# Performance work log

Hardware: AMD Instinct MI355X
Metric: run time of the kernel (lower is better)

The kernel has to match this reference:

```python
import jax, jax.numpy as jnp
import numpy as np

N_NODE = 100000
HIDDEN = 128
BATCH = 4096
SESS_LEN = 50


def setup_inputs() -> dict:
    key = jax.random.key(0)
    k1, k2, k3, k4, k5 = jax.random.split(key, 5)
    return {
        "item_embedding": jax.random.normal(k1, (N_NODE, HIDDEN), dtype=jnp.float32),
        "items": jax.random.randint(k2, (BATCH, SESS_LEN), 0, N_NODE, dtype=jnp.int64),
        "A": jax.random.uniform(k3, (BATCH, BATCH), dtype=jnp.float32),
        "D": jax.random.uniform(k4, (BATCH, BATCH), dtype=jnp.float32),
        "target_embedding": jax.random.normal(k5, (BATCH, 1, 2 * HIDDEN), dtype=jnp.float32),
    }


def reference(item_embedding, items, A, D, target_embedding):
    # Gather per-session item embeddings: (batch, sess_len, hidden)
    seq_h = item_embedding[items]
    # Sum over session positions -> (batch, hidden)
    relation_emb = jnp.sum(seq_h, axis=1)
    # DA = D @ A, then propagate: (batch, batch) @ (batch, hidden)
    DA = jnp.matmul(D, A)
    relation_emb = jnp.matmul(DA, relation_emb)
    # Row-wise L2 normalization (torch.norm(dim=-1))
    norm = jnp.linalg.norm(relation_emb, axis=-1, keepdims=True)
    return relation_emb / norm
```

## Files before the change

### kernel.cpp

```cpp
#include <hip/hip_runtime.h>
#include <hip/hip_bf16.h>

#define BATCH   4096
#define HIDDEN  128
#define SESS    50
#define KTOT    4096
#define NB      ((size_t)BATCH * HIDDEN)

#define MROWS   128
#define KSP     8
#define KQL     512
#define BK      32
#define NTL     (KQL / BK)
#define ABY     16384
#define BBY     8192
#define BUF     (ABY + BBY)
#define NBUF    5

typedef __bf16 bf16x8 __attribute__((ext_vector_type(8)));
typedef float  f32x4  __attribute__((ext_vector_type(4)));
typedef float  f32x2  __attribute__((ext_vector_type(2)));

__device__ __forceinline__ f32x4 mfma_bf16(bf16x8 a, bf16x8 b, f32x4 c) {
    return __builtin_amdgcn_mfma_f32_16x16x32_bf16(a, b, c, 0, 0, 0);
}

__device__ __forceinline__ void gload16(const void* g, void* l) {
    __builtin_amdgcn_global_load_lds(
        (const __attribute__((address_space(1))) void*)g,
        (__attribute__((address_space(3))) void*)l, 16, 0, 0);
}


__global__ __launch_bounds__(256)
void gather_sum_kernel(const float* __restrict__ emb,
                       const int* __restrict__ items32,
                       __bf16* __restrict__ ETp) {
    __shared__ int sidx[4][SESS];
    const int t  = threadIdx.x;
    const int b0 = blockIdx.x * 4;
    const bool is64 = (items32[1] | items32[3] | items32[5] | items32[7] |
                       items32[9] | items32[11] | items32[13] | items32[15]) == 0;
    if (t < 4 * SESS) {
        const int w_ = t / SESS, s_ = t % SESS;
        sidx[w_][s_] = is64
            ? (int)((const long long*)items32)[(long)(b0 + w_) * SESS + s_]
            : items32[(b0 + w_) * SESS + s_];
    }
    __syncthreads();
    const int w    = t >> 6;
    const int lane = t & 63;
    const int c    = lane & 31;
    const int h    = lane >> 5;
    f32x4 acc = {0.f, 0.f, 0.f, 0.f};
#pragma unroll
    for (int i = 0; i < 25; ++i) {
        acc += *(const f32x4*)(emb + (long)sidx[w][h + 2 * i] * HIDDEN + c * 4);
    }
#pragma unroll
    for (int j = 0; j < 4; ++j) acc[j] += __shfl_xor(acc[j], 32, 64);
    if (h == 0) {
        const int  b     = b0 + w;
        const long chunk = b >> 3;
        const int  swz   = (int)((chunk & 3) << 4);
        char* basep = (char*)ETp + chunk * 2048 + (b & 7) * 2;
        const int hi4 = (c >> 2) * 256;
#pragma unroll
        for (int j = 0; j < 4; ++j) {
            const int hl = 4 * (c & 3) + j;
            *(__bf16*)(basep + ((hi4 + hl * 16) ^ swz)) = (__bf16)acc[j];
        }
    }
}

__global__ __launch_bounds__(256, 1)
void gemm_mfma_kernel(const float* __restrict__ X,
                      const char* __restrict__ Bpk,
                      float* __restrict__ Tp) {
    __shared__ __align__(16) char lds[NBUF * BUF];
    const int tid  = threadIdx.x;
    const int w    = tid >> 6;
    const int lane = tid & 63;
    const int lo   = lane & 15;
    const int quad = lane >> 4;
    const int rowBase = blockIdx.x * MROWS;
    const int kq      = blockIdx.y;

    const int mh = w & 1;
    const int nh = w >> 1;
    const int akey = (lo & 7) << 4;
    const int bkey = quad << 4;

#define STG(t_, dst_) do {                                                   \
    _Pragma("unroll")                                                        \
    for (int ai_ = 0; ai_ < 4; ++ai_) {                                      \
        const int i_  = 4 * w + ai_;                                         \
        const int rl_ = 8 * i_ + (lane >> 3);          \
        gload16((const char*)X +                                             \
                    ((size_t)(rowBase + rl_) * KTOT + kq * KQL +             \
                     (size_t)(t_) * BK) * 4 +                                \
                    ((((lane & 7) * 16)) ^ ((rl_ & 7) << 4)),                \
                (dst_) + i_ * 1024);                                         \
    }                                                                        \
    _Pragma("unroll")                                                        \
    for (int bi_ = 0; bi_ < 2; ++bi_) {                                      \
        const int j_ = 2 * w + bi_;                                          \
        gload16(Bpk + ((size_t)(kq * 64 + (t_) * 4 + (j_ >> 1))) * 2048 +    \
                    (j_ & 1) * 1024 + lane * 16,                             \
                (dst_) + ABY + j_ * 1024);                                   \
    }                                                                        \
} while (0)

    f32x4 acc[4][4];
#pragma unroll
    for (int i = 0; i < 4; ++i)
#pragma unroll
        for (int j = 0; j < 4; ++j) acc[i][j] = (f32x4){0.f, 0.f, 0.f, 0.f};

#define KTL(cb_) do {                                                        \
    const char* Ab_ = (cb_);                                                 \
    const char* Bb_ = (cb_) + ABY + quad * 2048;                             \
    bf16x8 af_[4];                                                           \
    _Pragma("unroll")                                                        \
    for (int fm_ = 0; fm_ < 4; ++fm_) {                                      \
        const int rr_ = (mh * 64 + fm_ * 16 + lo) * 128;                     \
        const f32x4 a0_ = *(const f32x4*)(Ab_ + rr_ + ((quad * 32) ^ akey)); \
        const f32x4 a1_ =                                                    \
            *(const f32x4*)(Ab_ + rr_ + ((quad * 32 + 16) ^ akey));          \
        af_[fm_][0] = (__bf16)a0_[0]; af_[fm_][1] = (__bf16)a0_[1];          \
        af_[fm_][2] = (__bf16)a0_[2]; af_[fm_][3] = (__bf16)a0_[3];          \
        af_[fm_][4] = (__bf16)a1_[0]; af_[fm_][5] = (__bf16)a1_[1];          \
        af_[fm_][6] = (__bf16)a1_[2]; af_[fm_][7] = (__bf16)a1_[3];          \
    }                                                                        \
    bf16x8 bf_[4];                                                           \
    _Pragma("unroll")                                                        \
    for (int fn_ = 0; fn_ < 4; ++fn_)                                        \
        bf_[fn_] = *(const bf16x8*)(Bb_ +                                    \
            ((((nh * 4 + fn_) * 256) + lo * 16) ^ bkey));                    \
    _Pragma("unroll")                                                        \
    for (int fm_ = 0; fm_ < 4; ++fm_)                                        \
        _Pragma("unroll")                                                    \
        for (int fn_ = 0; fn_ < 4; ++fn_)                                    \
            acc[fm_][fn_] = mfma_bf16(af_[fm_], bf_[fn_], acc[fm_][fn_]);    \
} while (0)

    STG(0, lds + 0 * BUF);
    STG(1, lds + 1 * BUF);
    STG(2, lds + 2 * BUF);
    STG(3, lds + 3 * BUF);

#pragma unroll
    for (int t = 0; t < NTL; ++t) {
        if (t <= NTL - 4)
            asm volatile("s_waitcnt vmcnt(18)" ::: "memory");
        else if (t == NTL - 3)
            asm volatile("s_waitcnt vmcnt(12)" ::: "memory");
        else if (t == NTL - 2)
            asm volatile("s_waitcnt vmcnt(6)" ::: "memory");
        else
            asm volatile("s_waitcnt vmcnt(0)" ::: "memory");
        __builtin_amdgcn_s_barrier();
        __builtin_amdgcn_sched_barrier(0);
        if (t + 4 < NTL) STG(t + 4, lds + ((t + 4) % NBUF) * BUF);
        KTL(lds + (t % NBUF) * BUF);
        __builtin_amdgcn_sched_barrier(0);
    }
#undef STG
#undef KTL

    float* op = Tp + (size_t)kq * NB +
                (size_t)(rowBase + mh * 64) * HIDDEN + nh * 64;
#pragma unroll
    for (int fm = 0; fm < 4; ++fm)
#pragma unroll
        for (int r = 0; r < 4; ++r) {
            const int ro = (fm * 16 + quad * 4 + r) * HIDDEN;
#pragma unroll
            for (int fn = 0; fn < 4; ++fn)
                op[ro + fn * 16 + lo] = acc[fm][fn][r];
        }
}

__global__ __launch_bounds__(256)
void reduce8_kernel(const float* __restrict__ Tp, __bf16* __restrict__ TTp) {
    const size_t i = ((size_t)blockIdx.x * 256 + threadIdx.x) * 4;
    f32x4 a = *(const f32x4*)(Tp + i);
#pragma unroll
    for (int p = 1; p < KSP; ++p) a += *(const f32x4*)(Tp + p * NB + i);
    const int  b     = (int)(i >> 7);
    const int  h0    = (int)(i & 127);
    const long chunk = b >> 3;
    const int  swz   = (int)((chunk & 3) << 4);
    char* basep = (char*)TTp + chunk * 2048 + (b & 7) * 2;
#pragma unroll
    for (int j = 0; j < 4; ++j) {
        const int h = h0 + j;
        *(__bf16*)(basep + (((h >> 4) * 256 + (h & 15) * 16) ^ swz)) =
            (__bf16)a[j];
    }
}

__global__ __launch_bounds__(256)
void rednorm8_kernel(const float* __restrict__ Tp, float* __restrict__ out) {
    const int t    = threadIdx.x;
    const int w    = t >> 6;
    const int lane = t & 63;
    const int row  = blockIdx.x * 4 + w;
    const size_t base = (size_t)row * HIDDEN + lane * 2;
    f32x2 v = *(const f32x2*)(Tp + base);
#pragma unroll
    for (int p = 1; p < KSP; ++p) v += *(const f32x2*)(Tp + p * NB + base);
    float sq = v[0] * v[0] + v[1] * v[1];
#pragma unroll
    for (int m = 1; m < 64; m <<= 1) sq += __shfl_xor(sq, m, 64);
    const float s = rsqrtf(sq);
    f32x2 o = {v[0] * s, v[1] * s};
    *(f32x2*)(out + base) = o;
}

extern "C" void kernel_launch(void* const* d_in, const int* in_sizes, int n_in,
                              void* d_out, int out_size, void* d_ws, size_t ws_size,
                              hipStream_t stream) {
    const float* emb   = (const float*)d_in[0];
    const int*   items = (const int*)d_in[1];
    const float* A     = (const float*)d_in[2];
    const float* D     = (const float*)d_in[3];
    float* out = (float*)d_out;

    __bf16* ETp = (__bf16*)d_ws;
    __bf16* TTp = ETp + NB;
    float*  Tp  = (float*)(TTp + NB);

    gather_sum_kernel<<<BATCH / 4, 256, 0, stream>>>(emb, items, ETp);
    gemm_mfma_kernel<<<dim3(BATCH / MROWS, KSP), 256, 0, stream>>>(
        A, (const char*)ETp, Tp);
    reduce8_kernel<<<512, 256, 0, stream>>>(Tp, TTp);
    gemm_mfma_kernel<<<dim3(BATCH / MROWS, KSP), 256, 0, stream>>>(
        D, (const char*)TTp, Tp);
    rednorm8_kernel<<<BATCH / 4, 256, 0, stream>>>(Tp, out);
}
```

Baseline: 215.0 us.

## Fuse split-K reductions into GEMM kernels via per-row-block atomic counters

```diff
diff --git a/kernel.cpp b/kernel.cpp
--- a/kernel.cpp
+++ b/kernel.cpp
@@ -19,7 +19,6 @@
 
 typedef __bf16 bf16x8 __attribute__((ext_vector_type(8)));
 typedef float  f32x4  __attribute__((ext_vector_type(4)));
-typedef float  f32x2  __attribute__((ext_vector_type(2)));
 
 __device__ __forceinline__ f32x4 mfma_bf16(bf16x8 a, bf16x8 b, f32x4 c) {
     return __builtin_amdgcn_mfma_f32_16x16x32_bf16(a, b, c, 0, 0, 0);
@@ -35,10 +34,12 @@
 __global__ __launch_bounds__(256)
 void gather_sum_kernel(const float* __restrict__ emb,
                        const int* __restrict__ items32,
-                       __bf16* __restrict__ ETp) {
+                       __bf16* __restrict__ ETp,
+                       int* __restrict__ cnt) {
     __shared__ int sidx[4][SESS];
     const int t  = threadIdx.x;
     const int b0 = blockIdx.x * 4;
+    if (blockIdx.x == 0 && t < 64) cnt[t] = 0;
     const bool is64 = (items32[1] | items32[3] | items32[5] | items32[7] |
                        items32[9] | items32[11] | items32[13] | items32[15]) == 0;
     if (t < 4 * SESS) {
@@ -73,18 +74,23 @@
     }
 }
 
+template <int PHASE>
 __global__ __launch_bounds__(256, 1)
 void gemm_mfma_kernel(const float* __restrict__ X,
                       const char* __restrict__ Bpk,
-                      float* __restrict__ Tp) {
+                      float* __restrict__ Tp,
+                      __bf16* __restrict__ TTp,
+                      float* __restrict__ out,
+                      int* __restrict__ cnt) {
     __shared__ __align__(16) char lds[NBUF * BUF];
     const int tid  = threadIdx.x;
     const int w    = tid >> 6;
     const int lane = tid & 63;
     const int lo   = lane & 15;
     const int quad = lane >> 4;
-    const int rowBase = blockIdx.x * MROWS;
-    const int kq      = blockIdx.y;
+    const int mb   = blockIdx.x;
+    const int kq   = blockIdx.y;
+    const int rowBase = mb * MROWS;
 
     const int mh = w & 1;
     const int nh = w >> 1;
@@ -179,43 +185,66 @@
             for (int fn = 0; fn < 4; ++fn)
                 op[ro + fn * 16 + lo] = acc[fm][fn][r];
         }
-}
-
-__global__ __launch_bounds__(256)
-void reduce8_kernel(const float* __restrict__ Tp, __bf16* __restrict__ TTp) {
-    const size_t i = ((size_t)blockIdx.x * 256 + threadIdx.x) * 4;
-    f32x4 a = *(const f32x4*)(Tp + i);
-#pragma unroll
-    for (int p = 1; p < KSP; ++p) a += *(const f32x4*)(Tp + p * NB + i);
-    const int  b     = (int)(i >> 7);
-    const int  h0    = (int)(i & 127);
-    const long chunk = b >> 3;
-    const int  swz   = (int)((chunk & 3) << 4);
-    char* basep = (char*)TTp + chunk * 2048 + (b & 7) * 2;
-#pragma unroll
-    for (int j = 0; j < 4; ++j) {
-        const int h = h0 + j;
-        *(__bf16*)(basep + (((h >> 4) * 256 + (h & 15) * 16) ^ swz)) =
-            (__bf16)a[j];
-    }
-}
-
-__global__ __launch_bounds__(256)
-void rednorm8_kernel(const float* __restrict__ Tp, float* __restrict__ out) {
-    const int t    = threadIdx.x;
-    const int w    = t >> 6;
-    const int lane = t & 63;
-    const int row  = blockIdx.x * 4 + w;
-    const size_t base = (size_t)row * HIDDEN + lane * 2;
-    f32x2 v = *(const f32x2*)(Tp + base);
-#pragma unroll
-    for (int p = 1; p < KSP; ++p) v += *(const f32x2*)(Tp + p * NB + base);
-    float sq = v[0] * v[0] + v[1] * v[1];
-#pragma unroll
-    for (int m = 1; m < 64; m <<= 1) sq += __shfl_xor(sq, m, 64);
-    const float s = rsqrtf(sq);
-    f32x2 o = {v[0] * s, v[1] * s};
-    *(f32x2*)(out + base) = o;
+
+    __threadfence();
+    __syncthreads();
+    if (tid == 0) {
+        atomicAdd(&cnt[mb], 1);
+        while (__hip_atomic_load(&cnt[mb], __ATOMIC_ACQUIRE,
+                                 __HIP_MEMORY_SCOPE_AGENT) < KSP)
+            __builtin_amdgcn_s_sleep(2);
+    }
+    __syncthreads();
+    __threadfence();
+
+    const int r0 = rowBase + kq * 16;
+    if constexpr (PHASE == 1) {
+        for (int i = tid; i < 512; i += 256) {
+            const size_t off = (size_t)r0 * HIDDEN + (size_t)i * 4;
+            f32x4 a = *(const f32x4*)(Tp + off);
+#pragma unroll
+            for (int p = 1; p < KSP; ++p)
+                a += *(const f32x4*)(Tp + (size_t)p * NB + off);
+            const int  b     = (int)(off >> 7);
+            const int  h0    = (int)(off & 127);
+            const long chunk = b >> 3;
+            const int  swz   = (int)((chunk & 3) << 4);
+            char* basep = (char*)TTp + chunk * 2048 + (b & 7) * 2;
+#pragma unroll
+            for (int j = 0; j < 4; ++j) {
+                const int h = h0 + j;
+                *(__bf16*)(basep + (((h >> 4) * 256 + (h & 15) * 16) ^ swz)) =
+                    (__bf16)a[j];
+            }
+        }
+    } else {
+        float (*Cs)[132] = (float (*)[132])lds;
+        for (int i = tid; i < 512; i += 256) {
+            const size_t off = (size_t)r0 * HIDDEN + (size_t)i * 4;
+            f32x4 a = *(const f32x4*)(Tp + off);
+#pragma unroll
+            for (int p = 1; p < KSP; ++p)
+                a += *(const f32x4*)(Tp + (size_t)p * NB + off);
+            *(f32x4*)&Cs[(i * 4) >> 7][(i * 4) & 127] = a;
+        }
+        __syncthreads();
+        const int row = tid >> 4;
+        const int cg  = tid & 15;
+        const f32x4 c0 = *(const f32x4*)&Cs[row][cg * 8];
+        const f32x4 c1 = *(const f32x4*)&Cs[row][cg * 8 + 4];
+        float sq = c0[0] * c0[0] + c0[1] * c0[1] + c0[2] * c0[2] +
+                   c0[3] * c0[3] + c1[0] * c1[0] + c1[1] * c1[1] +
+                   c1[2] * c1[2] + c1[3] * c1[3];
+#pragma unroll
+        for (int m = 1; m < 16; m <<= 1) sq += __shfl_xor(sq, m, 64);
+        const float s = rsqrtf(sq);
+        float* opn = out + (size_t)(r0 + row) * HIDDEN + cg * 8;
+        f32x4 o0, o1;
+#pragma unroll
+        for (int j = 0; j < 4; ++j) { o0[j] = c0[j] * s; o1[j] = c1[j] * s; }
+        *(f32x4*)(opn)     = o0;
+        *(f32x4*)(opn + 4) = o1;
+    }
 }
 
 extern "C" void kernel_launch(void* const* d_in, const int* in_sizes, int n_in,
@@ -227,15 +256,14 @@
     const float* D     = (const float*)d_in[3];
     float* out = (float*)d_out;
 
-    __bf16* ETp = (__bf16*)d_ws;
+    int*    cnt = (int*)d_ws;
+    __bf16* ETp = (__bf16*)((char*)d_ws + 1024);
     __bf16* TTp = ETp + NB;
     float*  Tp  = (float*)(TTp + NB);
 
-    gather_sum_kernel<<<BATCH / 4, 256, 0, stream>>>(emb, items, ETp);
-    gemm_mfma_kernel<<<dim3(BATCH / MROWS, KSP), 256, 0, stream>>>(
-        A, (const char*)ETp, Tp);
-    reduce8_kernel<<<512, 256, 0, stream>>>(Tp, TTp);
-    gemm_mfma_kernel<<<dim3(BATCH / MROWS, KSP), 256, 0, stream>>>(
-        D, (const char*)TTp, Tp);
-    rednorm8_kernel<<<BATCH / 4, 256, 0, stream>>>(Tp, out);
-}
+    gather_sum_kernel<<<BATCH / 4, 256, 0, stream>>>(emb, items, ETp, cnt);
+    gemm_mfma_kernel<1><<<dim3(32, KSP), 256, 0, stream>>>(
+        A, (const char*)ETp, Tp, TTp, nullptr, cnt);
+    gemm_mfma_kernel<2><<<dim3(32, KSP), 256, 0, stream>>>(
+        D, (const char*)TTp, Tp, nullptr, out, cnt + 32);
+}
```

New measurement: 347.5 us. 1.62x slower.
